# Performance work log

Measured on AMD Instinct MI355X. Metric: run time of the kernel, lower is better.

## Reference

```python
import jax, jax.numpy as jnp
import numpy as np

GROUPS = 4
PPG = 16  # kv_channels // groups = 64 // 4
Q_CH = 256
KV_CH = 64


def setup_inputs() -> dict:
    key = jax.random.key(0)
    ks = jax.random.split(key, 7)
    N, T, L = 4, 64, 64
    q = jax.random.normal(ks[0], (N, L, L, Q_CH), dtype=jnp.float32)
    kv = jax.random.normal(ks[1], (N, T, L, L, KV_CH), dtype=jnp.float32)
    # torch nn.Linear weights, stored pre-transposed so y = x @ W
    s_q = 1.0 / np.sqrt(Q_CH)
    s_kv = 1.0 / np.sqrt(KV_CH)
    Wq = jax.random.uniform(ks[2], (Q_CH, KV_CH), jnp.float32, -s_q, s_q)
    Wk = jax.random.uniform(ks[3], (KV_CH, KV_CH), jnp.float32, -s_kv, s_kv)
    Wv = jax.random.uniform(ks[4], (KV_CH, KV_CH), jnp.float32, -s_kv, s_kv)
    Wout = jax.random.uniform(ks[5], (KV_CH, Q_CH), jnp.float32, -s_kv, s_kv)
    b_out = jax.random.uniform(ks[6], (Q_CH,), jnp.float32, -s_kv, s_kv)
    return {"q": q, "kv": kv, "Wq": Wq, "Wk": Wk, "Wv": Wv, "Wout": Wout, "b_out": b_out}


def reference(q, kv, Wq, Wk, Wv, Wout, b_out):
    N, L, _, _ = q.shape
    T = kv.shape[1]
    qh = (q @ Wq).reshape(N, L, L, GROUPS, PPG)                 # nijgc
    kh = (kv @ Wk).reshape(N, T, L, L, GROUPS, PPG)             # ntijgc
    vh = (kv @ Wv).reshape(N, T, L, L, GROUPS, PPG)             # ntijgc
    scale = 1.0 / jnp.sqrt(jnp.float32(PPG))
    attn = jnp.einsum('nijgc,ntijgc->ntijg', qh, kh) * scale    # scores over T per pixel
    attn = jax.nn.softmax(attn, axis=1)
    x = jnp.einsum('ntijg,ntijgc->nijgc', attn, vh).reshape(N, L, L, KV_CH)
    return x @ Wout + b_out
```

## Files before the change

### kernel.cpp

```cpp
#include <hip/hip_runtime.h>

typedef short short8 __attribute__((ext_vector_type(8)));
typedef float f32x4 __attribute__((ext_vector_type(4)));

__device__ __forceinline__ float bf2f(unsigned short u) {
  union { unsigned int i; float f; } v; v.i = ((unsigned int)u) << 16; return v.f;
}
__device__ __forceinline__ unsigned short f2bf(float f) {
  unsigned int x = __float_as_uint(f);
  unsigned int r = (x + 0x7fffu + ((x >> 16) & 1u)) >> 16;
  return (unsigned short)r;
}

typedef __attribute__((address_space(1))) void* gas_t;
typedef __attribute__((address_space(3))) void* las_t;
__device__ __forceinline__ void async16(const float* g, float* l) {
  __builtin_amdgcn_global_load_lds((gas_t)g, (las_t)l, 16, 0, 0);
}

template <int N>
__device__ __forceinline__ void wait_vm() {
  asm volatile("s_waitcnt vmcnt(%0)" :: "n"(N) : "memory");
  __builtin_amdgcn_sched_barrier(0);
}

__global__ __launch_bounds__(256) void prep_kernel(
    const float* __restrict__ Wq, const float* __restrict__ Wk,
    const float* __restrict__ Wv, const float* __restrict__ Wout,
    unsigned short* __restrict__ Afrag, unsigned short* __restrict__ WVOfrag) {
  const int b = blockIdx.x, tid = threadIdx.x;
  if (b < 256) {
    const int p = b, g = tid >> 6, d = tid & 63;
    float s = 0.f;
#pragma unroll
    for (int c = 0; c < 16; ++c)
      s += Wq[p * 64 + g * 16 + c] * Wk[d * 64 + g * 16 + c];
    s *= 0.25f;
    const int n = g * 64 + d, k = p;
    Afrag[(size_t)(k >> 5) * 8192 + n * 32 + (k & 31)] = f2bf(s);
  } else {
    const int row = b - 256, g = row >> 6, d = row & 63, q = tid;
    float s = 0.f;
#pragma unroll
    for (int c = 0; c < 16; ++c)
      s += Wv[d * 64 + g * 16 + c] * Wout[(g * 16 + c) * 256 + q];
    WVOfrag[(size_t)(row >> 5) * 8192 + q * 32 + (row & 31)] = f2bf(s);
  }
}

__global__ __launch_bounds__(256, 2) void fused_kernel(
    const float* __restrict__ q, const float* __restrict__ kv,
    const unsigned short* __restrict__ Afrag,
    const unsigned short* __restrict__ WVOfrag,
    const float* __restrict__ bias, float* __restrict__ Out) {
  __shared__ float kvbuf[5][2048];
  __shared__ unsigned short qk_s[32 * 264];
  __shared__ unsigned short qA_s[32 * 264];

  const int tid = threadIdx.x;
  const int wgid = blockIdx.x;
  const int w = tid >> 6, lane = tid & 63;
  const int m_l = lane & 15, quad = lane >> 4;

  const float* kvbase = kv + ((size_t)(wgid >> 7) << 24) +
                        ((size_t)((wgid >> 1) & 63) << 12) +
                        ((size_t)(wgid & 1) << 11);
  const int loff = w * 512 + lane * 4;

#pragma unroll
  for (int tt = 0; tt < 4; ++tt) {
    const float* src = kvbase + ((size_t)tt << 18) + loff;
    float* dst = &kvbuf[tt][loff];
    async16(src, dst);
    async16(src + 256, dst + 256);
  }

  {
    const float* qrow = q + (size_t)(wgid >> 1) * 16384 + (size_t)(wgid & 1) * 8192;
    const int r = tid >> 3, cc = (tid & 7) * 32;
    const float4* xp = (const float4*)(qrow + r * 256 + cc);
#pragma unroll
    for (int kk = 0; kk < 4; ++kk) {
      float4 x0 = xp[2 * kk], x1 = xp[2 * kk + 1];
      short8 vv;
      vv[0] = (short)f2bf(x0.x); vv[1] = (short)f2bf(x0.y);
      vv[2] = (short)f2bf(x0.z); vv[3] = (short)f2bf(x0.w);
      vv[4] = (short)f2bf(x1.x); vv[5] = (short)f2bf(x1.y);
      vv[6] = (short)f2bf(x1.z); vv[7] = (short)f2bf(x1.w);
      *(short8*)&qA_s[r * 264 + cc + kk * 8] = vv;
    }
  }
  __syncthreads();
  {
    f32x4 acc[2][4];
#pragma unroll
    for (int mt = 0; mt < 2; ++mt)
#pragma unroll
      for (int ntl = 0; ntl < 4; ++ntl) acc[mt][ntl] = (f32x4){0.f, 0.f, 0.f, 0.f};
#pragma unroll
    for (int ks = 0; ks < 8; ++ks) {
      short8 a0 = *(const short8*)&qA_s[m_l * 264 + ks * 32 + quad * 8];
      short8 a1 = *(const short8*)&qA_s[(16 + m_l) * 264 + ks * 32 + quad * 8];
#pragma unroll
      for (int ntl = 0; ntl < 4; ++ntl) {
        short8 bf = *(const short8*)(Afrag +
            ((size_t)ks * 256 + (w * 4 + ntl) * 16 + m_l) * 32 + quad * 8);
        acc[0][ntl] = __builtin_amdgcn_mfma_f32_16x16x32_bf16(a0, bf, acc[0][ntl], 0, 0, 0);
        acc[1][ntl] = __builtin_amdgcn_mfma_f32_16x16x32_bf16(a1, bf, acc[1][ntl], 0, 0, 0);
      }
    }
#pragma unroll
    for (int mt = 0; mt < 2; ++mt)
#pragma unroll
      for (int ntl = 0; ntl < 4; ++ntl) {
        const int col = (w * 4 + ntl) * 16 + m_l;
#pragma unroll
        for (int r4 = 0; r4 < 4; ++r4)
          qk_s[(mt * 16 + quad * 4 + r4) * 264 + col] = f2bf(acc[mt][ntl][r4]);
      }
  }
  __syncthreads();

  const int jl = tid >> 3, sub = tid & 7, g = sub >> 1, h = sub & 1;

  float qf[32];
#pragma unroll
  for (int c = 0; c < 8; ++c) {
    const int rot = (c + jl) & 7;
    uint2 u = *(const uint2*)&qk_s[jl * 264 + g * 64 + h * 32 + rot * 4];
    qf[4 * c + 0] = bf2f((unsigned short)(u.x & 0xffffu));
    qf[4 * c + 1] = bf2f((unsigned short)(u.x >> 16));
    qf[4 * c + 2] = bf2f((unsigned short)(u.y & 0xffffu));
    qf[4 * c + 3] = bf2f((unsigned short)(u.y >> 16));
  }

  float yac[32];
#pragma unroll
  for (int c = 0; c < 32; ++c) yac[c] = 0.f;
  float lsum = 0.f;

  auto stepT = [&](int slot) {
    const float* row = &kvbuf[slot][jl * 64 + h * 32];
    float s = 0.f;
    float4 cv[8];
#pragma unroll
    for (int c = 0; c < 8; ++c) {
      const int rot = (c + jl) & 7;
      cv[c] = *(const float4*)(row + rot * 4);
      s = fmaf(cv[c].x, qf[4 * c + 0], s);
      s = fmaf(cv[c].y, qf[4 * c + 1], s);
      s = fmaf(cv[c].z, qf[4 * c + 2], s);
      s = fmaf(cv[c].w, qf[4 * c + 3], s);
    }
    const float so = __shfl_xor(s, 1, 64);
    const float p = __expf(s + so);
    lsum += p;
#pragma unroll
    for (int c = 0; c < 8; ++c) {
      yac[4 * c + 0] = fmaf(p, cv[c].x, yac[4 * c + 0]);
      yac[4 * c + 1] = fmaf(p, cv[c].y, yac[4 * c + 1]);
      yac[4 * c + 2] = fmaf(p, cv[c].z, yac[4 * c + 2]);
      yac[4 * c + 3] = fmaf(p, cv[c].w, yac[4 * c + 3]);
    }
  };

  int sb = 0, si = 4;
#pragma unroll 1
  for (int t = 0; t < 60; ++t) {
    wait_vm<6>();
    const float* src = kvbase + ((size_t)(t + 4) << 18) + loff;
    float* dst = &kvbuf[si][loff];
    async16(src, dst);
    async16(src + 256, dst + 256);
    stepT(sb);
    sb = (sb == 4) ? 0 : sb + 1;
    si = (si == 4) ? 0 : si + 1;
  }
  wait_vm<6>(); stepT(0);
  wait_vm<4>(); stepT(1);
  wait_vm<2>(); stepT(2);
  wait_vm<0>(); stepT(3);

  {
    const float inv = 1.f / lsum;
#pragma unroll
    for (int c = 0; c < 8; ++c) {
      const int rot = (c + jl) & 7;
      uint2 pk;
      pk.x = (unsigned int)f2bf(yac[4 * c + 0] * inv) |
             ((unsigned int)f2bf(yac[4 * c + 1] * inv) << 16);
      pk.y = (unsigned int)f2bf(yac[4 * c + 2] * inv) |
             ((unsigned int)f2bf(yac[4 * c + 3] * inv) << 16);
      *(uint2*)&qk_s[jl * 264 + g * 64 + h * 32 + rot * 4] = pk;
    }
  }
  __syncthreads();

  {
    f32x4 acc[2][4];
#pragma unroll
    for (int mt = 0; mt < 2; ++mt)
#pragma unroll
      for (int ntl = 0; ntl < 4; ++ntl) acc[mt][ntl] = (f32x4){0.f, 0.f, 0.f, 0.f};
#pragma unroll
    for (int ks = 0; ks < 8; ++ks) {
      short8 a0 = *(const short8*)&qk_s[m_l * 264 + ks * 32 + quad * 8];
      short8 a1 = *(const short8*)&qk_s[(16 + m_l) * 264 + ks * 32 + quad * 8];
#pragma unroll
      for (int ntl = 0; ntl < 4; ++ntl) {
        short8 bf = *(const short8*)(WVOfrag +
            ((size_t)ks * 256 + (w * 4 + ntl) * 16 + m_l) * 32 + quad * 8);
        acc[0][ntl] = __builtin_amdgcn_mfma_f32_16x16x32_bf16(a0, bf, acc[0][ntl], 0, 0, 0);
        acc[1][ntl] = __builtin_amdgcn_mfma_f32_16x16x32_bf16(a1, bf, acc[1][ntl], 0, 0, 0);
      }
    }
    float* outb = Out + (size_t)(wgid >> 1) * 16384 + (size_t)(wgid & 1) * 8192;
#pragma unroll
    for (int mt = 0; mt < 2; ++mt)
#pragma unroll
      for (int ntl = 0; ntl < 4; ++ntl) {
        const int col = (w * 4 + ntl) * 16 + m_l;
        const float bb = bias[col];
#pragma unroll
        for (int r4 = 0; r4 < 4; ++r4)
          outb[(size_t)(mt * 16 + quad * 4 + r4) * 256 + col] = acc[mt][ntl][r4] + bb;
      }
  }
}

extern "C" void kernel_launch(void* const* d_in, const int* in_sizes, int n_in,
                              void* d_out, int out_size, void* d_ws,
                              size_t ws_size, hipStream_t stream) {
  const float* q    = (const float*)d_in[0];
  const float* kv   = (const float*)d_in[1];
  const float* Wq   = (const float*)d_in[2];
  const float* Wk   = (const float*)d_in[3];
  const float* Wv   = (const float*)d_in[4];
  const float* Wout = (const float*)d_in[5];
  const float* bout = (const float*)d_in[6];

  unsigned short* ws      = (unsigned short*)d_ws;
  unsigned short* Afrag   = ws;
  unsigned short* WVOfrag = ws + 65536;

  hipLaunchKernelGGL(prep_kernel, dim3(512), dim3(256), 0, stream,
                     Wq, Wk, Wv, Wout, Afrag, WVOfrag);
  hipLaunchKernelGGL(fused_kernel, dim3(512), dim3(256), 0, stream,
                     q, kv, Afrag, WVOfrag, bout, (float*)d_out);
}
```

Baseline: 387.3 us.

## Deepen kv prefetch ring, preload weight fragments, avoid vmcnt-draining barriers

Grows the kv LDS ring from 5 to 7 slots so six timesteps of async global-to-LDS loads stay in flight, and adjusts the wait counts and tail steps to match. The q and qk staging buffers are merged into one LDS buffer to free space for the larger ring. The q rows and the Afrag weight fragments are loaded into registers before the kv prefetch is issued. __syncthreads is replaced with a barrier that waits only on lgkmcnt, so the kv prefetch is not drained at the prologue barriers. The goal is to hide global-memory latency in a stream that is far below peak bandwidth. In exchange, the 128 registers held by the preloaded fragments add VGPR pressure and could cause spills.

```diff
diff --git a/kernel.cpp b/kernel.cpp
--- a/kernel.cpp
+++ b/kernel.cpp
@@ -22,6 +22,12 @@
 __device__ __forceinline__ void wait_vm() {
   asm volatile("s_waitcnt vmcnt(%0)" :: "n"(N) : "memory");
   __builtin_amdgcn_sched_barrier(0);
+}
+
+__device__ __forceinline__ void barrier_lgkm() {
+  asm volatile("s_waitcnt lgkmcnt(0)" ::: "memory");
+  __builtin_amdgcn_sched_barrier(0);
+  __builtin_amdgcn_s_barrier();
 }
 
 __global__ __launch_bounds__(256) void prep_kernel(
@@ -53,9 +59,8 @@
     const unsigned short* __restrict__ Afrag,
     const unsigned short* __restrict__ WVOfrag,
     const float* __restrict__ bias, float* __restrict__ Out) {
-  __shared__ float kvbuf[5][2048];
-  __shared__ unsigned short qk_s[32 * 264];
-  __shared__ unsigned short qA_s[32 * 264];
+  __shared__ float kvbuf[7][2048];
+  __shared__ unsigned short qbuf[32 * 264];
 
   const int tid = threadIdx.x;
   const int wgid = blockIdx.x;
@@ -67,30 +72,43 @@
                         ((size_t)(wgid & 1) << 11);
   const int loff = w * 512 + lane * 4;
 
-#pragma unroll
-  for (int tt = 0; tt < 4; ++tt) {
+  const float* qrow = q + (size_t)(wgid >> 1) * 16384 + (size_t)(wgid & 1) * 8192;
+  const int r = tid >> 3, cc = (tid & 7) * 32;
+  const float4* xp = (const float4*)(qrow + r * 256 + cc);
+  float4 xv[8];
+#pragma unroll
+  for (int kk = 0; kk < 8; ++kk) xv[kk] = xp[kk];
+  __builtin_amdgcn_sched_barrier(0);
+
+  short8 bfr[8][4];
+#pragma unroll
+  for (int ks = 0; ks < 8; ++ks)
+#pragma unroll
+    for (int ntl = 0; ntl < 4; ++ntl)
+      bfr[ks][ntl] = *(const short8*)(Afrag +
+          ((size_t)ks * 256 + (w * 4 + ntl) * 16 + m_l) * 32 + quad * 8);
+  __builtin_amdgcn_sched_barrier(0);
+
+#pragma unroll
+  for (int tt = 0; tt < 6; ++tt) {
     const float* src = kvbase + ((size_t)tt << 18) + loff;
     float* dst = &kvbuf[tt][loff];
     async16(src, dst);
     async16(src + 256, dst + 256);
   }
-
-  {
-    const float* qrow = q + (size_t)(wgid >> 1) * 16384 + (size_t)(wgid & 1) * 8192;
-    const int r = tid >> 3, cc = (tid & 7) * 32;
-    const float4* xp = (const float4*)(qrow + r * 256 + cc);
-#pragma unroll
-    for (int kk = 0; kk < 4; ++kk) {
-      float4 x0 = xp[2 * kk], x1 = xp[2 * kk + 1];
-      short8 vv;
-      vv[0] = (short)f2bf(x0.x); vv[1] = (short)f2bf(x0.y);
-      vv[2] = (short)f2bf(x0.z); vv[3] = (short)f2bf(x0.w);
-      vv[4] = (short)f2bf(x1.x); vv[5] = (short)f2bf(x1.y);
-      vv[6] = (short)f2bf(x1.z); vv[7] = (short)f2bf(x1.w);
-      *(short8*)&qA_s[r * 264 + cc + kk * 8] = vv;
-    }
-  }
-  __syncthreads();
+  __builtin_amdgcn_sched_barrier(0);
+
+#pragma unroll
+  for (int kk = 0; kk < 4; ++kk) {
+    float4 x0 = xv[2 * kk], x1 = xv[2 * kk + 1];
+    short8 vv;
+    vv[0] = (short)f2bf(x0.x); vv[1] = (short)f2bf(x0.y);
+    vv[2] = (short)f2bf(x0.z); vv[3] = (short)f2bf(x0.w);
+    vv[4] = (short)f2bf(x1.x); vv[5] = (short)f2bf(x1.y);
+    vv[6] = (short)f2bf(x1.z); vv[7] = (short)f2bf(x1.w);
+    *(short8*)&qbuf[r * 264 + cc + kk * 8] = vv;
+  }
+  barrier_lgkm();
   {
     f32x4 acc[2][4];
 #pragma unroll
@@ -99,16 +117,15 @@
       for (int ntl = 0; ntl < 4; ++ntl) acc[mt][ntl] = (f32x4){0.f, 0.f, 0.f, 0.f};
 #pragma unroll
     for (int ks = 0; ks < 8; ++ks) {
-      short8 a0 = *(const short8*)&qA_s[m_l * 264 + ks * 32 + quad * 8];
-      short8 a1 = *(const short8*)&qA_s[(16 + m_l) * 264 + ks * 32 + quad * 8];
-#pragma unroll
-      for (int ntl = 0; ntl < 4; ++ntl) {
-        short8 bf = *(const short8*)(Afrag +
-            ((size_t)ks * 256 + (w * 4 + ntl) * 16 + m_l) * 32 + quad * 8);
-        acc[0][ntl] = __builtin_amdgcn_mfma_f32_16x16x32_bf16(a0, bf, acc[0][ntl], 0, 0, 0);
-        acc[1][ntl] = __builtin_amdgcn_mfma_f32_16x16x32_bf16(a1, bf, acc[1][ntl], 0, 0, 0);
-      }
-    }
+      short8 a0 = *(const short8*)&qbuf[m_l * 264 + ks * 32 + quad * 8];
+      short8 a1 = *(const short8*)&qbuf[(16 + m_l) * 264 + ks * 32 + quad * 8];
+#pragma unroll
+      for (int ntl = 0; ntl < 4; ++ntl) {
+        acc[0][ntl] = __builtin_amdgcn_mfma_f32_16x16x32_bf16(a0, bfr[ks][ntl], acc[0][ntl], 0, 0, 0);
+        acc[1][ntl] = __builtin_amdgcn_mfma_f32_16x16x32_bf16(a1, bfr[ks][ntl], acc[1][ntl], 0, 0, 0);
+      }
+    }
+    barrier_lgkm();
 #pragma unroll
     for (int mt = 0; mt < 2; ++mt)
 #pragma unroll
@@ -116,10 +133,10 @@
         const int col = (w * 4 + ntl) * 16 + m_l;
 #pragma unroll
         for (int r4 = 0; r4 < 4; ++r4)
-          qk_s[(mt * 16 + quad * 4 + r4) * 264 + col] = f2bf(acc[mt][ntl][r4]);
-      }
-  }
-  __syncthreads();
+          qbuf[(mt * 16 + quad * 4 + r4) * 264 + col] = f2bf(acc[mt][ntl][r4]);
+      }
+  }
+  barrier_lgkm();
 
   const int jl = tid >> 3, sub = tid & 7, g = sub >> 1, h = sub & 1;
 
@@ -127,7 +144,7 @@
 #pragma unroll
   for (int c = 0; c < 8; ++c) {
     const int rot = (c + jl) & 7;
-    uint2 u = *(const uint2*)&qk_s[jl * 264 + g * 64 + h * 32 + rot * 4];
+    uint2 u = *(const uint2*)&qbuf[jl * 264 + g * 64 + h * 32 + rot * 4];
     qf[4 * c + 0] = bf2f((unsigned short)(u.x & 0xffffu));
     qf[4 * c + 1] = bf2f((unsigned short)(u.x >> 16));
     qf[4 * c + 2] = bf2f((unsigned short)(u.y & 0xffffu));
@@ -164,22 +181,24 @@
     }
   };
 
-  int sb = 0, si = 4;
+  int sb = 0, si = 6;
 #pragma unroll 1
-  for (int t = 0; t < 60; ++t) {
-    wait_vm<6>();
-    const float* src = kvbase + ((size_t)(t + 4) << 18) + loff;
+  for (int t = 0; t < 58; ++t) {
+    wait_vm<10>();
+    const float* src = kvbase + ((size_t)(t + 6) << 18) + loff;
     float* dst = &kvbuf[si][loff];
     async16(src, dst);
     async16(src + 256, dst + 256);
     stepT(sb);
-    sb = (sb == 4) ? 0 : sb + 1;
-    si = (si == 4) ? 0 : si + 1;
-  }
-  wait_vm<6>(); stepT(0);
-  wait_vm<4>(); stepT(1);
-  wait_vm<2>(); stepT(2);
-  wait_vm<0>(); stepT(3);
+    sb = (sb == 6) ? 0 : sb + 1;
+    si = (si == 6) ? 0 : si + 1;
+  }
+  wait_vm<10>(); stepT(2);
+  wait_vm<8>();  stepT(3);
+  wait_vm<6>();  stepT(4);
+  wait_vm<4>();  stepT(5);
+  wait_vm<2>();  stepT(6);
+  wait_vm<0>();  stepT(0);
 
   {
     const float inv = 1.f / lsum;
@@ -191,10 +210,10 @@
              ((unsigned int)f2bf(yac[4 * c + 1] * inv) << 16);
       pk.y = (unsigned int)f2bf(yac[4 * c + 2] * inv) |
              ((unsigned int)f2bf(yac[4 * c + 3] * inv) << 16);
-      *(uint2*)&qk_s[jl * 264 + g * 64 + h * 32 + rot * 4] = pk;
-    }
-  }
-  __syncthreads();
+      *(uint2*)&qbuf[jl * 264 + g * 64 + h * 32 + rot * 4] = pk;
+    }
+  }
+  barrier_lgkm();
 
   {
     f32x4 acc[2][4];
@@ -204,8 +223,8 @@
       for (int ntl = 0; ntl < 4; ++ntl) acc[mt][ntl] = (f32x4){0.f, 0.f, 0.f, 0.f};
 #pragma unroll
     for (int ks = 0; ks < 8; ++ks) {
-      short8 a0 = *(const short8*)&qk_s[m_l * 264 + ks * 32 + quad * 8];
-      short8 a1 = *(const short8*)&qk_s[(16 + m_l) * 264 + ks * 32 + quad * 8];
+      short8 a0 = *(const short8*)&qbuf[m_l * 264 + ks * 32 + quad * 8];
+      short8 a1 = *(const short8*)&qbuf[(16 + m_l) * 264 + ks * 32 + quad * 8];
 #pragma unroll
       for (int ntl = 0; ntl < 4; ++ntl) {
         short8 bf = *(const short8*)(WVOfrag +
```

New measurement: 395.4 us. +2.1%, slower.
